# Kernel optimization log

Hardware: AMD Instinct MI355X
Metric: run time of the kernel (lower is better)

## Reference

```python
import jax, jax.numpy as jnp
import numpy as np

B = 8192          # batch
FEAT = 14 * 14 * (16 + 4)  # 3920 features per image
NUM_CLASSES = 10
REPS = 8          # CX+RY repetitions in the filter circuit


def _filter_probs(p):
    """Analytic output distribution of the 4-qubit filter circuit.
    p: (..., 4) pixel angles [p0, p1, p2, p3].
    Circuit: RY(p_i) on qubit i, then 8x [CX(0,1); RY(p0,0)], measure all.
    Qubits 2,3 stay in product state; evolve (q0,q1) as a real 2x2 amplitude
    grid a[q0, q1]. Output index = q0*8 + q1*4 + q2*2 + q3 (Qiskit bitstring
    reversed as in the torch source).
    """
    h = 0.5 * p
    c, s = jnp.cos(h), jnp.sin(h)
    v0 = jnp.stack([c[..., 0], s[..., 0]], axis=-1)
    v1 = jnp.stack([c[..., 1], s[..., 1]], axis=-1)
    a = v0[..., :, None] * v1[..., None, :]        # (..., 2, 2) amplitudes a[q0,q1]
    c0, s0 = c[..., 0], s[..., 0]
    R0 = jnp.stack([jnp.stack([c0, -s0], axis=-1),
                    jnp.stack([s0,  c0], axis=-1)], axis=-2)  # RY(p0) matrix
    for _ in range(REPS):
        # CX(control=q0, target=q1): flip q1 where q0 == 1
        a = jnp.stack([a[..., 0, :], a[..., 1, ::-1]], axis=-2)
        # RY(p0) on q0
        a = jnp.einsum('...ik,...kj->...ij', R0, a)
    P01 = a * a                                    # joint probs over (q0, q1)
    p2 = s[..., 2] ** 2                            # P(q2 = 1)
    p3 = s[..., 3] ** 2                            # P(q3 = 1)
    P2 = jnp.stack([1.0 - p2, p2], axis=-1)
    P3 = jnp.stack([1.0 - p3, p3], axis=-1)
    P = (P01[..., :, :, None, None]
         * P2[..., None, None, :, None]
         * P3[..., None, None, None, :])           # (..., q0, q1, q2, q3)
    return P.reshape(P.shape[:-4] + (16,))


def _sampler_probs(tl, br):
    """2-qubit sampler with all weights = 0: the two CX(0,1) cancel, so the
    state is RY(tl)|0> x RY(br)|0>. Output index = q0*2 + q1."""
    s0 = jnp.sin(0.5 * tl) ** 2   # P(q0 = 1)
    s1 = jnp.sin(0.5 * br) ** 2   # P(q1 = 1)
    return jnp.stack([(1 - s0) * (1 - s1), (1 - s0) * s1,
                      s0 * (1 - s1), s0 * s1], axis=-1)


def setup_inputs() -> dict:
    key = jax.random.key(0)
    k1, k2 = jax.random.split(key)
    x = jax.random.uniform(k1, (B, 1, 28, 28), dtype=jnp.float32)
    fc_w = jax.random.normal(k2, (NUM_CLASSES, FEAT), dtype=jnp.float32) * (FEAT ** -0.5)
    fc_b = jnp.zeros((NUM_CLASSES,), dtype=jnp.float32)
    return {"x": x, "fc_w": fc_w, "fc_b": fc_b}


def reference(x, fc_w, fc_b):
    b = x.shape[0]
    # (b, 14, 14, 2, 2) patches; patch[u, v] = img[2i+u, 2j+v]
    patches = x.reshape(b, 14, 2, 14, 2).transpose(0, 1, 3, 2, 4)
    p = patches.reshape(b, 196, 4)                 # [p0, p1, p2, p3] per patch
    filter_feats = _filter_probs(p).reshape(b, -1)            # (b, 196*16)
    sampler_feats = _sampler_probs(patches[..., 0, 0],
                                   patches[..., 1, 1]).reshape(b, -1)  # (b, 196*4)
    feats = jnp.concatenate([filter_feats, sampler_feats], axis=-1)
    logits = feats @ fc_w.T + fc_b
    return jax.nn.log_softmax(logits, axis=-1)
```

## Files before the change

### kernel.cpp

```cpp
#include <hip/hip_runtime.h>
#include <hip/hip_bf16.h>

typedef float v2f __attribute__((ext_vector_type(2)));
typedef short short8 __attribute__((ext_vector_type(8)));
typedef float f32x4 __attribute__((ext_vector_type(4)));

#define NCLS  10
#define FEATN 3920
#define GIMG  8
#define RSTR  532

__device__ __forceinline__ unsigned packbf(float a, float b) {
    __hip_bfloat162 h = __float22bfloat162_rn(float2{a, b});
    unsigned u; __builtin_memcpy(&u, &h, 4); return u;
}

__device__ __forceinline__ void fastsc(float v, float& s, float& c) {
    const float r = v * 0.07957747154594767f;
#if __has_builtin(__builtin_amdgcn_sinf)
    s = __builtin_amdgcn_sinf(r);
    c = __builtin_amdgcn_cosf(r);
#else
    s = __sinf(0.5f * v);
    c = __cosf(0.5f * v);
#endif
}

__global__ void conv_w(const float* __restrict__ fc_w, __hip_bfloat16* __restrict__ ws) {
    const int id = blockIdx.x * 256 + threadIdx.x;
    if (id >= 123 * 512) return;
    const int kb = id >> 9, r = id & 511, l = r >> 3, j0 = r & 7;
    const int n  = l & 15;
    const int kk = kb * 32 + ((l >> 4) << 3) + j0;
    float w = 0.f;
    if (n < NCLS) {
        const int t    = (kk < 2880) ? kk / 960 : 3;
        const int base = 960 * t;
        const int P0   = 48 * t;
        const int np   = (t == 3) ? 52 : 48;
        const int u    = kk - base;
        int korig = -1;
        if (u < np * 16) {
            korig = 16 * (P0 + (u >> 4)) + (u & 15);
        } else {
            const int v = u - np * 16;
            if (v < np * 4) korig = 3136 + 4 * (P0 + (v >> 2)) + (v & 3);
        }
        if (korig >= 0) w = fc_w[n * FEATN + korig];
    }
    ws[id] = __float2bfloat16(w);
}

__global__ __launch_bounds__(256, 4)
void quanv_mfma(const float* __restrict__ x,
                const short* __restrict__ wsb,
                const float* __restrict__ fc_b,
                float* __restrict__ out) {
    __shared__ __align__(16) unsigned lds[GIMG * RSTR];
    const int tid  = threadIdx.x;
    const int lane = tid & 63;
    const int wave = tid >> 6;
    const int img0 = blockIdx.x * GIMG;
    const float* base = x + (size_t)img0 * 784;
    const int am  = lane & 15;
    const int ach = lane >> 4;
    const unsigned aoff = (unsigned)((am & 7) * RSTR + ach * 4);

    float2 pix[4][4];
    int lpv[4], qv[4];
    bool act[4];
    #pragma unroll
    for (int t = 0; t < 4; ++t) {
        const int np = (t == 3) ? 52 : 48;
        const int P0 = 48 * t;
        const bool a = tid < np * 4;
        const int tt = a ? tid : 0;
        const int q  = tt / np;
        const int lp = tt - q * np;
        const int p  = P0 + lp;
        const int pi = p / 14, pj = p - pi * 14;
        const int off = pi * 56 + pj * 2;
        const float* iA = base + (size_t)(2 * q) * 784;
        pix[t][0] = *reinterpret_cast<const float2*>(iA + off);
        pix[t][1] = *reinterpret_cast<const float2*>(iA + off + 28);
        pix[t][2] = *reinterpret_cast<const float2*>(iA + 784 + off);
        pix[t][3] = *reinterpret_cast<const float2*>(iA + 784 + off + 28);
        lpv[t] = lp; qv[t] = q; act[t] = a;
    }

    f32x4 acc = {0.f, 0.f, 0.f, 0.f};

    #pragma unroll
    for (int t = 0; t < 4; ++t) {
        const int np  = (t == 3) ? 52 : 48;
        const int nkb = (t == 3) ? 33 : 30;
        const int kbb = 30 * t;

        if (act[t]) {
            const float2 tA = pix[t][0], bA = pix[t][1];
            const float2 tB = pix[t][2], bB = pix[t][3];
            float sA0,cA0,sA1,cA1,sA2,cA2,sA3,cA3;
            float sB0,cB0,sB1,cB1,sB2,cB2,sB3,cB3;
            fastsc(tA.x, sA0, cA0); fastsc(tA.y, sA1, cA1);
            fastsc(bA.x, sA2, cA2); fastsc(bA.y, sA3, cA3);
            fastsc(tB.x, sB0, cB0); fastsc(tB.y, sB1, cB1);
            fastsc(bB.x, sB2, cB2); fastsc(bB.y, sB3, cB3);

            const v2f c0 = {cA0, cB0}, s0 = {sA0, sB0};
            const v2f c1 = {cA1, cB1}, s1 = {sA1, sB1};
            v2f a00 = c0 * c1, a01 = c0 * s1, a10 = s0 * c1, a11 = s0 * s1;
            #pragma unroll
            for (int r = 0; r < 8; ++r) {
                const v2f b10 = a11, b11 = a10;
                const v2f n00 = c0 * a00 - s0 * b10;
                const v2f n01 = c0 * a01 - s0 * b11;
                const v2f n10 = s0 * a00 + c0 * b10;
                const v2f n11 = s0 * a01 + c0 * b11;
                a00 = n00; a01 = n01; a10 = n10; a11 = n11;
            }
            v2f P2[4];
            P2[0] = a00 * a00; P2[1] = a01 * a01; P2[2] = a10 * a10; P2[3] = a11 * a11;
            const v2f t2c = {cA2*cA2, cB2*cB2}, t2s = {sA2*sA2, sB2*sB2};
            const v2f t3c = {cA3*cA3, cB3*cB3}, t3s = {sA3*sA3, sB3*sB3};
            v2f T[4];
            T[0] = t2c * t3c; T[1] = t2c * t3s; T[2] = t2s * t3c; T[3] = t2s * t3s;

            unsigned dA[8], dB[8];
            #pragma unroll
            for (int m = 0; m < 4; ++m) {
                const v2f f0 = P2[m] * T[0], f1 = P2[m] * T[1];
                const v2f f2 = P2[m] * T[2], f3 = P2[m] * T[3];
                dA[2*m]   = packbf(f0.x, f1.x); dA[2*m+1] = packbf(f2.x, f3.x);
                dB[2*m]   = packbf(f0.y, f1.y); dB[2*m+1] = packbf(f2.y, f3.y);
            }
            const v2f sa = s0 * s0, sb = t3s;
            const v2f na = 1.0f - sa, nb = 1.0f - sb;
            const v2f e0 = na * nb, e1 = na * sb, e2 = sa * nb, e3 = sa * sb;

            const int lp = lpv[t], q = qv[t];
            unsigned* rowA = lds + (2 * q) * RSTR;
            unsigned* rowB = rowA + RSTR;
            *reinterpret_cast<uint4*>(rowA + lp * 8)     = uint4{dA[0], dA[1], dA[2], dA[3]};
            *reinterpret_cast<uint4*>(rowA + lp * 8 + 4) = uint4{dA[4], dA[5], dA[6], dA[7]};
            *reinterpret_cast<uint2*>(rowA + np * 8 + lp * 2) =
                uint2{packbf(e0.x, e1.x), packbf(e2.x, e3.x)};
            *reinterpret_cast<uint4*>(rowB + lp * 8)     = uint4{dB[0], dB[1], dB[2], dB[3]};
            *reinterpret_cast<uint4*>(rowB + lp * 8 + 4) = uint4{dB[4], dB[5], dB[6], dB[7]};
            *reinterpret_cast<uint2*>(rowB + np * 8 + lp * 2) =
                uint2{packbf(e0.y, e1.y), packbf(e2.y, e3.y)};
        }
        if (t == 3 && tid < 64)
            lds[(tid >> 3) * RSTR + 520 + (tid & 7)] = 0u;
        __syncthreads();

        for (int kb = wave; kb < nkb; kb += 4) {
            const short8 a = *reinterpret_cast<const short8*>(lds + aoff + kb * 16);
            const short8 b = *reinterpret_cast<const short8*>(wsb + (size_t)(kbb + kb) * 512 + lane * 8);
            acc = __builtin_amdgcn_mfma_f32_16x16x32_bf16(a, b, acc, 0, 0, 0);
        }
        __syncthreads();
    }

    float* f = reinterpret_cast<float*>(lds);
    f[wave * 256 +   0 + lane] = acc[0];
    f[wave * 256 +  64 + lane] = acc[1];
    f[wave * 256 + 128 + lane] = acc[2];
    f[wave * 256 + 192 + lane] = acc[3];
    __syncthreads();
    if (tid < GIMG * NCLS) {
        const int g = tid / NCLS, c = tid - g * NCLS;
        const int li = ((g >> 2) << 4) + c;
        const int ri = (g & 3) << 6;
        float v = f[ri + li] + f[256 + ri + li] + f[512 + ri + li] + f[768 + ri + li];
        f[1024 + tid] = v + fc_b[c];
    }
    __syncthreads();
    if (tid < GIMG * NCLS) {
        const int g = tid / NCLS, c = tid - g * NCLS;
        const float* lg = f + 1024 + g * NCLS;
        float m = -1e30f;
        #pragma unroll
        for (int k = 0; k < NCLS; ++k) m = fmaxf(m, lg[k]);
        float ss = 0.f;
        #pragma unroll
        for (int k = 0; k < NCLS; ++k) ss += __expf(lg[k] - m);
        out[(size_t)(img0 + g) * NCLS + c] = lg[c] - m - __logf(ss);
    }
}

extern "C" void kernel_launch(void* const* d_in, const int* in_sizes, int n_in,
                              void* d_out, int out_size, void* d_ws, size_t ws_size,
                              hipStream_t stream) {
    const float* x    = (const float*)d_in[0];
    const float* fc_w = (const float*)d_in[1];
    const float* fc_b = (const float*)d_in[2];
    float* out = (float*)d_out;

    conv_w<<<246, 256, 0, stream>>>(fc_w, (__hip_bfloat16*)d_ws);

    const int B = in_sizes[0] / 784;
    const int grid = B / GIMG;
    quanv_mfma<<<grid, 256, 0, stream>>>(x, (const short*)d_ws, fc_b, out);
}
```

Before: 84.84 us.

## Fuse weight bf16 conversion into main kernel and prefetch next pixel chunk

Removes the separate conv_w launch that repacked fc_w into bf16 MFMA layout. The main kernel now reads fp32 fc_w directly in the MFMA loop, remaps indices on the fly and converts to bf16 per use. It also loads the next chunk's pixels just before the barrier instead of holding all four chunks up front, which lowers register pressure. The cost is twice the global weight bytes per block (fp32 instead of bf16) plus extra address and conversion ALU work inside the inner loop.

```diff
diff --git a/kernel.cpp b/kernel.cpp
--- a/kernel.cpp
+++ b/kernel.cpp
@@ -26,36 +26,11 @@
 #endif
 }
 
-__global__ void conv_w(const float* __restrict__ fc_w, __hip_bfloat16* __restrict__ ws) {
-    const int id = blockIdx.x * 256 + threadIdx.x;
-    if (id >= 123 * 512) return;
-    const int kb = id >> 9, r = id & 511, l = r >> 3, j0 = r & 7;
-    const int n  = l & 15;
-    const int kk = kb * 32 + ((l >> 4) << 3) + j0;
-    float w = 0.f;
-    if (n < NCLS) {
-        const int t    = (kk < 2880) ? kk / 960 : 3;
-        const int base = 960 * t;
-        const int P0   = 48 * t;
-        const int np   = (t == 3) ? 52 : 48;
-        const int u    = kk - base;
-        int korig = -1;
-        if (u < np * 16) {
-            korig = 16 * (P0 + (u >> 4)) + (u & 15);
-        } else {
-            const int v = u - np * 16;
-            if (v < np * 4) korig = 3136 + 4 * (P0 + (v >> 2)) + (v & 3);
-        }
-        if (korig >= 0) w = fc_w[n * FEATN + korig];
-    }
-    ws[id] = __float2bfloat16(w);
-}
-
 __global__ __launch_bounds__(256, 4)
-void quanv_mfma(const float* __restrict__ x,
-                const short* __restrict__ wsb,
-                const float* __restrict__ fc_b,
-                float* __restrict__ out) {
+void quanv_all(const float* __restrict__ x,
+               const float* __restrict__ fc_w,
+               const float* __restrict__ fc_b,
+               float* __restrict__ out) {
     __shared__ __align__(16) unsigned lds[GIMG * RSTR];
     const int tid  = threadIdx.x;
     const int lane = tid & 63;
@@ -65,40 +40,36 @@
     const int am  = lane & 15;
     const int ach = lane >> 4;
     const unsigned aoff = (unsigned)((am & 7) * RSTR + ach * 4);
-
-    float2 pix[4][4];
-    int lpv[4], qv[4];
-    bool act[4];
-    #pragma unroll
-    for (int t = 0; t < 4; ++t) {
-        const int np = (t == 3) ? 52 : 48;
-        const int P0 = 48 * t;
-        const bool a = tid < np * 4;
-        const int tt = a ? tid : 0;
-        const int q  = tt / np;
-        const int lp = tt - q * np;
-        const int p  = P0 + lp;
-        const int pi = p / 14, pj = p - pi * 14;
-        const int off = pi * 56 + pj * 2;
-        const float* iA = base + (size_t)(2 * q) * 784;
-        pix[t][0] = *reinterpret_cast<const float2*>(iA + off);
-        pix[t][1] = *reinterpret_cast<const float2*>(iA + off + 28);
-        pix[t][2] = *reinterpret_cast<const float2*>(iA + 784 + off);
-        pix[t][3] = *reinterpret_cast<const float2*>(iA + 784 + off + 28);
-        lpv[t] = lp; qv[t] = q; act[t] = a;
-    }
+    const bool bnv = am < NCLS;
+    const float* wrow = fc_w + (size_t)(bnv ? am : 0) * FEATN;
+    const int ach8 = ach * 8;
 
     f32x4 acc = {0.f, 0.f, 0.f, 0.f};
 
+    float2 pc[4], pn[4];
+    int lpC, qC; bool actC;
+    {
+        actC = tid < 48 * 4;
+        const int tt = actC ? tid : 0;
+        qC = tt / 48; lpC = tt - qC * 48;
+        const int pi = lpC / 14, pj = lpC - pi * 14;
+        const int off = pi * 56 + pj * 2;
+        const float* iA = base + (size_t)(2 * qC) * 784;
+        pc[0] = *reinterpret_cast<const float2*>(iA + off);
+        pc[1] = *reinterpret_cast<const float2*>(iA + off + 28);
+        pc[2] = *reinterpret_cast<const float2*>(iA + 784 + off);
+        pc[3] = *reinterpret_cast<const float2*>(iA + 784 + off + 28);
+    }
+
     #pragma unroll
     for (int t = 0; t < 4; ++t) {
-        const int np  = (t == 3) ? 52 : 48;
-        const int nkb = (t == 3) ? 33 : 30;
-        const int kbb = 30 * t;
+        const int np   = (t == 3) ? 52 : 48;
+        const int nkb  = (t == 3) ? 33 : 30;
+        const int np16 = np * 16, np20 = np * 20;
+        const int fb   = 768 * t, sb = 3136 + 192 * t;
 
-        if (act[t]) {
-            const float2 tA = pix[t][0], bA = pix[t][1];
-            const float2 tB = pix[t][2], bB = pix[t][3];
+        if (actC) {
+            const float2 tA = pc[0], bA = pc[1], tB = pc[2], bB = pc[3];
             float sA0,cA0,sA1,cA1,sA2,cA2,sA3,cA3;
             float sB0,cB0,sB1,cB1,sB2,cB2,sB3,cB3;
             fastsc(tA.x, sA0, cA0); fastsc(tA.y, sA1, cA1);
@@ -133,32 +104,58 @@
                 dA[2*m]   = packbf(f0.x, f1.x); dA[2*m+1] = packbf(f2.x, f3.x);
                 dB[2*m]   = packbf(f0.y, f1.y); dB[2*m+1] = packbf(f2.y, f3.y);
             }
-            const v2f sa = s0 * s0, sb = t3s;
-            const v2f na = 1.0f - sa, nb = 1.0f - sb;
-            const v2f e0 = na * nb, e1 = na * sb, e2 = sa * nb, e3 = sa * sb;
+            const v2f sa = s0 * s0, sb2 = t3s;
+            const v2f na = 1.0f - sa, nb = 1.0f - sb2;
+            const v2f e0 = na * nb, e1 = na * sb2, e2 = sa * nb, e3 = sa * sb2;
 
-            const int lp = lpv[t], q = qv[t];
-            unsigned* rowA = lds + (2 * q) * RSTR;
+            unsigned* rowA = lds + (2 * qC) * RSTR;
             unsigned* rowB = rowA + RSTR;
-            *reinterpret_cast<uint4*>(rowA + lp * 8)     = uint4{dA[0], dA[1], dA[2], dA[3]};
-            *reinterpret_cast<uint4*>(rowA + lp * 8 + 4) = uint4{dA[4], dA[5], dA[6], dA[7]};
-            *reinterpret_cast<uint2*>(rowA + np * 8 + lp * 2) =
+            *reinterpret_cast<uint4*>(rowA + lpC * 8)     = uint4{dA[0], dA[1], dA[2], dA[3]};
+            *reinterpret_cast<uint4*>(rowA + lpC * 8 + 4) = uint4{dA[4], dA[5], dA[6], dA[7]};
+            *reinterpret_cast<uint2*>(rowA + np * 8 + lpC * 2) =
                 uint2{packbf(e0.x, e1.x), packbf(e2.x, e3.x)};
-            *reinterpret_cast<uint4*>(rowB + lp * 8)     = uint4{dB[0], dB[1], dB[2], dB[3]};
-            *reinterpret_cast<uint4*>(rowB + lp * 8 + 4) = uint4{dB[4], dB[5], dB[6], dB[7]};
-            *reinterpret_cast<uint2*>(rowB + np * 8 + lp * 2) =
+            *reinterpret_cast<uint4*>(rowB + lpC * 8)     = uint4{dB[0], dB[1], dB[2], dB[3]};
+            *reinterpret_cast<uint4*>(rowB + lpC * 8 + 4) = uint4{dB[4], dB[5], dB[6], dB[7]};
+            *reinterpret_cast<uint2*>(rowB + np * 8 + lpC * 2) =
                 uint2{packbf(e0.y, e1.y), packbf(e2.y, e3.y)};
         }
         if (t == 3 && tid < 64)
             lds[(tid >> 3) * RSTR + 520 + (tid & 7)] = 0u;
+
+        int lpN = 0, qN = 0; bool actN = false;
+        if (t < 3) {
+            const int npN = (t + 1 == 3) ? 52 : 48;
+            actN = tid < npN * 4;
+            const int tt = actN ? tid : 0;
+            qN = tt / npN; lpN = tt - qN * npN;
+            const int p = 48 * (t + 1) + lpN;
+            const int pi = p / 14, pj = p - pi * 14;
+            const int off = pi * 56 + pj * 2;
+            const float* iA = base + (size_t)(2 * qN) * 784;
+            pn[0] = *reinterpret_cast<const float2*>(iA + off);
+            pn[1] = *reinterpret_cast<const float2*>(iA + off + 28);
+            pn[2] = *reinterpret_cast<const float2*>(iA + 784 + off);
+            pn[3] = *reinterpret_cast<const float2*>(iA + 784 + off + 28);
+        }
         __syncthreads();
 
         for (int kb = wave; kb < nkb; kb += 4) {
             const short8 a = *reinterpret_cast<const short8*>(lds + aoff + kb * 16);
-            const short8 b = *reinterpret_cast<const short8*>(wsb + (size_t)(kbb + kb) * 512 + lane * 8);
+            const int u = kb * 32 + ach8;
+            const bool val = bnv && (u < np20);
+            const int addr = val ? ((u < np16) ? fb + u : sb + (u - np16)) : 0;
+            float4 wa = *reinterpret_cast<const float4*>(wrow + addr);
+            float4 wb = *reinterpret_cast<const float4*>(wrow + addr + 4);
+            if (!val) { wa = float4{0.f,0.f,0.f,0.f}; wb = float4{0.f,0.f,0.f,0.f}; }
+            const uint4 bu{packbf(wa.x, wa.y), packbf(wa.z, wa.w),
+                           packbf(wb.x, wb.y), packbf(wb.z, wb.w)};
+            short8 b; __builtin_memcpy(&b, &bu, 16);
             acc = __builtin_amdgcn_mfma_f32_16x16x32_bf16(a, b, acc, 0, 0, 0);
         }
         __syncthreads();
+
+        pc[0] = pn[0]; pc[1] = pn[1]; pc[2] = pn[2]; pc[3] = pn[3];
+        lpC = lpN; qC = qN; actC = actN;
     }
 
     float* f = reinterpret_cast<float*>(lds);
@@ -195,10 +192,7 @@
     const float* fc_w = (const float*)d_in[1];
     const float* fc_b = (const float*)d_in[2];
     float* out = (float*)d_out;
-
-    conv_w<<<246, 256, 0, stream>>>(fc_w, (__hip_bfloat16*)d_ws);
-
     const int B = in_sizes[0] / 784;
     const int grid = B / GIMG;
-    quanv_mfma<<<grid, 256, 0, stream>>>(x, (const short*)d_ws, fc_b, out);
+    quanv_all<<<grid, 256, 0, stream>>>(x, fc_w, fc_b, out);
 }
```

Measured after the change: 89.29 us. 5.2% more time.
